# Kernel tuning notes

Measured on AMD Instinct MI355X. Metric: run time of the kernel, lower is better.

## Reference

```python
import jax, jax.numpy as jnp
import numpy as np

N_NODES = 50000
N_EDGES = 800000
D_IN = 96
D_OUT = 96
K_ORDER = 3


def setup_inputs() -> dict:
    key = jax.random.key(0)
    k1, k2, k3, k4, k5 = jax.random.split(key, 5)
    rows = jax.random.randint(k1, (N_EDGES,), 0, N_NODES, dtype=jnp.int64 if jax.config.jax_enable_x64 else jnp.int32)
    cols = jax.random.randint(k2, (N_EDGES,), 0, N_NODES, dtype=jnp.int64 if jax.config.jax_enable_x64 else jnp.int32)
    vals = jax.random.uniform(k3, (N_EDGES,), dtype=jnp.float32) * (1.0 / 16.0)  # ~sym-normalized weights
    H = jax.random.normal(k4, (N_NODES, D_IN), dtype=jnp.float32)
    W = jax.random.normal(k5, (D_IN, D_OUT), dtype=jnp.float32) * (1.0 / np.sqrt(D_IN))
    bias = jnp.zeros((D_OUT,), dtype=jnp.float32)
    return {"rows": rows, "cols": cols, "vals": vals, "H": H, "W": W, "bias": bias}


def reference(rows, cols, vals, H, W, bias):
    n = H.shape[0]

    def spmm(X):  # L @ X via gather-multiply-scatter over COO edges
        return jax.ops.segment_sum(vals[:, None] * X[cols], rows, num_segments=n)

    def ln_mm(X):  # (2L - I) @ X
        return 2.0 * spmm(X) - X

    # k = 0 term: T_0 = H
    H_out = H @ W
    # k = 1 term: T_1 = (2L - I) H  (differentiable, as in torch code)
    T_prev = H
    T_curr = ln_mm(H)
    H_out = H_out + T_curr @ W
    # k >= 2: recurrence computed under no_grad in the original -> stop_gradient
    for _ in range(2, K_ORDER + 1):
        T_next = jax.lax.stop_gradient(2.0 * ln_mm(T_curr) - T_prev)
        H_out = H_out + T_next @ W
        T_prev, T_curr = T_curr, T_next
    return H_out + bias
```

## Files before the change

kernel.cpp:

```cpp
#include <hip/hip_runtime.h>
#include <hip/hip_fp16.h>

#define NN 50000
#define NE 800000
#define D  96
#define NB_SCAN 196

typedef unsigned int   uint32;
typedef unsigned short uint16;
typedef short v8s __attribute__((ext_vector_type(8)));
typedef float v4f __attribute__((ext_vector_type(4)));

__device__ inline uint16 f32_to_bf16(float f) {
    uint32 u = __float_as_uint(f);
    u += 0x7FFF + ((u >> 16) & 1);
    return (uint16)(u >> 16);
}
__device__ inline float bf16_to_f32(uint16 h) {
    return __uint_as_float(((uint32)h) << 16);
}

__global__ void to_bf16(const float4* __restrict__ X, ushort4* __restrict__ Xb, int n4) {
    int i = blockIdx.x * blockDim.x + threadIdx.x;
    if (i < n4) {
        float4 v = X[i];
        ushort4 o;
        o.x = f32_to_bf16(v.x); o.y = f32_to_bf16(v.y);
        o.z = f32_to_bf16(v.z); o.w = f32_to_bf16(v.w);
        Xb[i] = o;
    }
}

__global__ void zero_counts(int* __restrict__ counts) {
    int i = blockIdx.x * blockDim.x + threadIdx.x;
    if (i < NN) counts[i] = 0;
}

__global__ void hist_slots(const int* __restrict__ rows, int* __restrict__ counts,
                           int* __restrict__ slot) {
    int e = blockIdx.x * blockDim.x + threadIdx.x;
    if (e < NE) slot[e] = atomicAdd(&counts[rows[e]], 1);
}

__global__ void scan_p1(const int* __restrict__ counts, int* __restrict__ partials) {
    __shared__ int red[256];
    int t = threadIdx.x;
    int i = blockIdx.x * 256 + t;
    red[t] = (i < NN) ? counts[i] : 0;
    __syncthreads();
    for (int off = 128; off > 0; off >>= 1) {
        if (t < off) red[t] += red[t + off];
        __syncthreads();
    }
    if (t == 0) partials[blockIdx.x] = red[0];
}

__global__ void scan_p2(int* __restrict__ partials) {
    __shared__ int sh[256];
    int t = threadIdx.x;
    int v = (t < NB_SCAN) ? partials[t] : 0;
    sh[t] = v;
    __syncthreads();
    for (int off = 1; off < 256; off <<= 1) {
        int u = (t >= off) ? sh[t - off] : 0;
        __syncthreads();
        sh[t] += u;
        __syncthreads();
    }
    if (t < NB_SCAN) partials[t] = sh[t] - v;
}

__global__ void scan_p3(const int* __restrict__ counts, const int* __restrict__ partials,
                        int* __restrict__ row_ptr) {
    __shared__ int sh[256];
    int t = threadIdx.x;
    int i = blockIdx.x * 256 + t;
    int v = (i < NN) ? counts[i] : 0;
    sh[t] = v;
    __syncthreads();
    for (int off = 1; off < 256; off <<= 1) {
        int u = (t >= off) ? sh[t - off] : 0;
        __syncthreads();
        sh[t] += u;
        __syncthreads();
    }
    int excl = sh[t] - v + partials[blockIdx.x];
    if (i < NN) row_ptr[i] = excl;
    if (i == NN - 1) row_ptr[NN] = excl + v;
}

__global__ void fill_edges(const int* __restrict__ rows, const int* __restrict__ cols,
                           const float* __restrict__ vals, const int* __restrict__ row_ptr,
                           const int* __restrict__ slot, uint32* __restrict__ edges) {
    int e = blockIdx.x * blockDim.x + threadIdx.x;
    if (e < NE) {
        int p = row_ptr[rows[e]] + slot[e];
        __half_raw hr = __half_raw(__float2half(vals[e]));
        edges[p] = (uint32)(cols[e] & 0xFFFF) | ((uint32)hr.x << 16);
    }
}

__global__ void spmm(const int* __restrict__ row_ptr, const uint32* __restrict__ edges,
                     const uint16* __restrict__ Xb, const float* __restrict__ A,
                     const float* __restrict__ B, float* __restrict__ Y,
                     uint16* __restrict__ Yb,
                     float scale, float ca, float cb, int n_nodes) {
    int tid  = threadIdx.x;
    int lane = tid & 31;
    int g    = tid >> 5;
    int r = blockIdx.x * 8 + g;
    if (r >= n_nodes) return;
    bool act = lane < 24;

    float4 acc = make_float4(0.f, 0.f, 0.f, 0.f);
    if (act) {
        float4 av = ((const float4*)(A + (size_t)r * D))[lane];
        float4 bv = ((const float4*)(B + (size_t)r * D))[lane];
        acc.x = ca * av.x + cb * bv.x;
        acc.y = ca * av.y + cb * bv.y;
        acc.z = ca * av.z + cb * bv.z;
        acc.w = ca * av.w + cb * bv.w;
    }

    int s = row_ptr[r];
    int e = row_ptr[r + 1];
    int i = s;
    for (; i + 3 < e; i += 4) {
        uint32 e0 = edges[i], e1 = edges[i+1], e2 = edges[i+2], e3 = edges[i+3];
        ushort4 x0, x1, x2, x3;
        x0.x=x0.y=x0.z=x0.w=0; x1=x0; x2=x0; x3=x0;
        if (act) {
            x0 = ((const ushort4*)(Xb + (size_t)(e0 & 0xFFFF) * D))[lane];
            x1 = ((const ushort4*)(Xb + (size_t)(e1 & 0xFFFF) * D))[lane];
            x2 = ((const ushort4*)(Xb + (size_t)(e2 & 0xFFFF) * D))[lane];
            x3 = ((const ushort4*)(Xb + (size_t)(e3 & 0xFFFF) * D))[lane];
        }
        __half_raw h0, h1, h2, h3;
        h0.x = (uint16)(e0 >> 16); h1.x = (uint16)(e1 >> 16);
        h2.x = (uint16)(e2 >> 16); h3.x = (uint16)(e3 >> 16);
        float v0 = scale * __half2float(__half(h0));
        float v1 = scale * __half2float(__half(h1));
        float v2 = scale * __half2float(__half(h2));
        float v3 = scale * __half2float(__half(h3));
        acc.x += v0*bf16_to_f32(x0.x) + v1*bf16_to_f32(x1.x) + v2*bf16_to_f32(x2.x) + v3*bf16_to_f32(x3.x);
        acc.y += v0*bf16_to_f32(x0.y) + v1*bf16_to_f32(x1.y) + v2*bf16_to_f32(x2.y) + v3*bf16_to_f32(x3.y);
        acc.z += v0*bf16_to_f32(x0.z) + v1*bf16_to_f32(x1.z) + v2*bf16_to_f32(x2.z) + v3*bf16_to_f32(x3.z);
        acc.w += v0*bf16_to_f32(x0.w) + v1*bf16_to_f32(x1.w) + v2*bf16_to_f32(x2.w) + v3*bf16_to_f32(x3.w);
    }
    for (; i < e; ++i) {
        uint32 e0 = edges[i];
        __half_raw h0; h0.x = (uint16)(e0 >> 16);
        float v0 = scale * __half2float(__half(h0));
        if (act) {
            ushort4 x0 = ((const ushort4*)(Xb + (size_t)(e0 & 0xFFFF) * D))[lane];
            acc.x += v0 * bf16_to_f32(x0.x);
            acc.y += v0 * bf16_to_f32(x0.y);
            acc.z += v0 * bf16_to_f32(x0.z);
            acc.w += v0 * bf16_to_f32(x0.w);
        }
    }
    if (act) {
        if (Y) ((float4*)(Y + (size_t)r * D))[lane] = acc;
        if (Yb) {
            ushort4 ob;
            ob.x = f32_to_bf16(acc.x); ob.y = f32_to_bf16(acc.y);
            ob.z = f32_to_bf16(acc.z); ob.w = f32_to_bf16(acc.w);
            ((ushort4*)(Yb + (size_t)r * D))[lane] = ob;
        }
    }
}

__global__ void wfrag_prep(const float* __restrict__ W, uint16* __restrict__ Wfrag) {
    int bt = blockIdx.x;
    int nt = bt / 3, kc = bt % 3;
    int lane = threadIdx.x;
    int col = nt * 16 + (lane & 15);
    int kbase = kc * 32 + (lane >> 4) * 8;
    uint16 tmp[8];
    #pragma unroll
    for (int j = 0; j < 8; ++j) tmp[j] = f32_to_bf16(W[(kbase + j) * D + col]);
    uint32* dst = (uint32*)(Wfrag + ((size_t)bt * 64 + lane) * 8);
    const uint32* src = (const uint32*)tmp;
    #pragma unroll
    for (int j = 0; j < 4; ++j) dst[j] = src[j];
}

__global__ void mfma_gemm(const uint16* __restrict__ Sb, const uint16* __restrict__ Wfrag,
                          const float* __restrict__ bias, float* __restrict__ out) {
    int tid   = threadIdx.x;
    int lane  = tid & 63;
    int wv    = blockIdx.x * (blockDim.x >> 6) + (tid >> 6);
    int nwv   = gridDim.x * (blockDim.x >> 6);
    int col   = lane & 15;
    int quad  = lane >> 4;

    v8s wf[6][3];
    #pragma unroll
    for (int nt = 0; nt < 6; ++nt)
        #pragma unroll
        for (int kc = 0; kc < 3; ++kc)
            wf[nt][kc] = ((const v8s*)Wfrag)[(nt * 3 + kc) * 64 + lane];

    float bi[6];
    #pragma unroll
    for (int nt = 0; nt < 6; ++nt) bi[nt] = bias[nt * 16 + col];

    for (int s = wv; s < NN / 16; s += nwv) {
        int r0 = s * 16;
        const uint16* arow = Sb + (size_t)(r0 + col) * D + quad * 8;
        v8s a0 = *((const v8s*)(arow));
        v8s a1 = *((const v8s*)(arow + 32));
        v8s a2 = *((const v8s*)(arow + 64));
        v4f acc[6];
        #pragma unroll
        for (int nt = 0; nt < 6; ++nt) {
            v4f c = {0.f, 0.f, 0.f, 0.f};
            c = __builtin_amdgcn_mfma_f32_16x16x32_bf16(a0, wf[nt][0], c, 0, 0, 0);
            c = __builtin_amdgcn_mfma_f32_16x16x32_bf16(a1, wf[nt][1], c, 0, 0, 0);
            c = __builtin_amdgcn_mfma_f32_16x16x32_bf16(a2, wf[nt][2], c, 0, 0, 0);
            acc[nt] = c;
        }
        #pragma unroll
        for (int nt = 0; nt < 6; ++nt) {
            float* o = out + (size_t)(r0 + quad * 4) * D + nt * 16 + col;
            o[0 * D] = acc[nt][0] + bi[nt];
            o[1 * D] = acc[nt][1] + bi[nt];
            o[2 * D] = acc[nt][2] + bi[nt];
            o[3 * D] = acc[nt][3] + bi[nt];
        }
    }
}

extern "C" void kernel_launch(void* const* d_in, const int* in_sizes, int n_in,
                              void* d_out, int out_size, void* d_ws, size_t ws_size,
                              hipStream_t stream) {
    const int*   rows = (const int*)d_in[0];
    const int*   cols = (const int*)d_in[1];
    const float* vals = (const float*)d_in[2];
    const float* H    = (const float*)d_in[3];
    const float* W    = (const float*)d_in[4];
    const float* bias = (const float*)d_in[5];
    float* out = (float*)d_out;

    char* ws = (char*)d_ws;
    float*  buf0     = (float*)ws;   ws += (size_t)NN * D * 4;
    float*  T2       = (float*)ws;   ws += (size_t)NN * D * 4;
    uint16* Hb       = (uint16*)ws;  ws += (size_t)NN * D * 2;
    uint16* T1b      = (uint16*)ws;  ws += (size_t)NN * D * 2;
    uint16* T2b      = (uint16*)ws;  ws += (size_t)NN * D * 2;
    uint32* edges    = (uint32*)ws;  ws += (size_t)NE * 4;
    uint16* Wfrag    = (uint16*)ws;  ws += (size_t)18 * 64 * 8 * 2;
    int*    counts   = (int*)ws;     ws += (size_t)NN * 4;
    int*    row_ptr  = (int*)ws;     ws += (size_t)(NN + 1) * 4;
    int*    partials = (int*)ws;     ws += 256 * 4;
    int*    slot     = (int*)buf0;
    float*  T1       = buf0;
    uint16* Sb       = T1b;

    const int nb  = (NN + 255) / 256;
    const int eb  = (NE + 255) / 256;
    const int n4  = NN * D / 4;
    const int cb4 = (n4 + 255) / 256;

    to_bf16<<<cb4, 256, 0, stream>>>((const float4*)H, (ushort4*)Hb, n4);
    wfrag_prep<<<18, 64, 0, stream>>>(W, Wfrag);

    zero_counts<<<nb, 256, 0, stream>>>(counts);
    hist_slots<<<eb, 256, 0, stream>>>(rows, counts, slot);
    scan_p1<<<NB_SCAN, 256, 0, stream>>>(counts, partials);
    scan_p2<<<1, 256, 0, stream>>>(partials);
    scan_p3<<<NB_SCAN, 256, 0, stream>>>(counts, partials, row_ptr);
    fill_edges<<<eb, 256, 0, stream>>>(rows, cols, vals, row_ptr, slot, edges);

    const int sb = (NN + 7) / 8;

    spmm<<<sb, 256, 0, stream>>>(row_ptr, edges, Hb, H, H, T1, T1b, 2.0f, -1.0f, 0.0f, NN);
    spmm<<<sb, 256, 0, stream>>>(row_ptr, edges, T1b, T1, H, T2, T2b, 4.0f, -2.0f, -1.0f, NN);
    spmm<<<sb, 256, 0, stream>>>(row_ptr, edges, T2b, H, T2, (float*)nullptr, Sb, 4.0f, 1.0f, -1.0f, NN);
    mfma_gemm<<<391, 256, 0, stream>>>(Sb, Wfrag, bias, out);
}
```

Baseline: 258.5 us.

## Keep Chebyshev intermediates in bf16 only and merge prep and scan kernels

The three SpMM passes now read their residual operands (H, T1, T2) from the bf16 copies and write only bf16 outputs, so the fp32 intermediate buffers are gone. This roughly halves the dense row traffic per pass. Separately, the H-to-bf16 conversion, count zeroing and W fragment prep are fused into one launch, and scan phases 2 and 3 are merged so each block rescans the partials itself. The cost is extra rounding error, because the recurrence's subtracted terms are now bf16 rather than fp32, and some redundant partial-scan work in every block.

Result: faster. 240.7 us (-6.9%).

```diff
diff --git a/kernel.cpp b/kernel.cpp
--- a/kernel.cpp
+++ b/kernel.cpp
@@ -5,6 +5,9 @@
 #define NE 800000
 #define D  96
 #define NB_SCAN 196
+#define N4 (NN * D / 4)
+#define CB4 ((N4 + 255) / 256)
+#define WFRAG_BLKS 5
 
 typedef unsigned int   uint32;
 typedef unsigned short uint16;
@@ -20,20 +23,39 @@
     return __uint_as_float(((uint32)h) << 16);
 }
 
-__global__ void to_bf16(const float4* __restrict__ X, ushort4* __restrict__ Xb, int n4) {
-    int i = blockIdx.x * blockDim.x + threadIdx.x;
-    if (i < n4) {
-        float4 v = X[i];
-        ushort4 o;
-        o.x = f32_to_bf16(v.x); o.y = f32_to_bf16(v.y);
-        o.z = f32_to_bf16(v.z); o.w = f32_to_bf16(v.w);
-        Xb[i] = o;
-    }
-}
-
-__global__ void zero_counts(int* __restrict__ counts) {
-    int i = blockIdx.x * blockDim.x + threadIdx.x;
-    if (i < NN) counts[i] = 0;
+__global__ void prep(const float4* __restrict__ H, ushort4* __restrict__ Hb,
+                     const float* __restrict__ W, uint16* __restrict__ Wfrag,
+                     int* __restrict__ counts) {
+    int b = blockIdx.x;
+    int t = threadIdx.x;
+    if (b < CB4) {
+        int i = b * 256 + t;
+        if (i < N4) {
+            float4 v = H[i];
+            ushort4 o;
+            o.x = f32_to_bf16(v.x); o.y = f32_to_bf16(v.y);
+            o.z = f32_to_bf16(v.z); o.w = f32_to_bf16(v.w);
+            Hb[i] = o;
+        }
+    } else if (b < CB4 + NB_SCAN) {
+        int i = (b - CB4) * 256 + t;
+        if (i < NN) counts[i] = 0;
+    } else {
+        int idx = (b - CB4 - NB_SCAN) * 256 + t;
+        if (idx < 18 * 64) {
+            int bt = idx >> 6, lane = idx & 63;
+            int nt = bt / 3, kc = bt % 3;
+            int col = nt * 16 + (lane & 15);
+            int kbase = kc * 32 + (lane >> 4) * 8;
+            uint16 tmp[8];
+            #pragma unroll
+            for (int j = 0; j < 8; ++j) tmp[j] = f32_to_bf16(W[(kbase + j) * D + col]);
+            uint32* dst = (uint32*)(Wfrag + ((size_t)bt * 64 + lane) * 8);
+            const uint32* src = (const uint32*)tmp;
+            #pragma unroll
+            for (int j = 0; j < 4; ++j) dst[j] = src[j];
+        }
+    }
 }
 
 __global__ void hist_slots(const int* __restrict__ rows, int* __restrict__ counts,
@@ -55,25 +77,20 @@
     if (t == 0) partials[blockIdx.x] = red[0];
 }
 
-__global__ void scan_p2(int* __restrict__ partials) {
+__global__ void scan_p23(const int* __restrict__ counts, const int* __restrict__ partials,
+                         int* __restrict__ row_ptr) {
+    __shared__ int pp[256];
     __shared__ int sh[256];
     int t = threadIdx.x;
-    int v = (t < NB_SCAN) ? partials[t] : 0;
-    sh[t] = v;
+    pp[t] = (t < NB_SCAN) ? partials[t] : 0;
     __syncthreads();
     for (int off = 1; off < 256; off <<= 1) {
-        int u = (t >= off) ? sh[t - off] : 0;
-        __syncthreads();
-        sh[t] += u;
-        __syncthreads();
-    }
-    if (t < NB_SCAN) partials[t] = sh[t] - v;
-}
-
-__global__ void scan_p3(const int* __restrict__ counts, const int* __restrict__ partials,
-                        int* __restrict__ row_ptr) {
-    __shared__ int sh[256];
-    int t = threadIdx.x;
+        int u = (t >= off) ? pp[t - off] : 0;
+        __syncthreads();
+        pp[t] += u;
+        __syncthreads();
+    }
+    int blk_off = (blockIdx.x == 0) ? 0 : pp[blockIdx.x - 1];
     int i = blockIdx.x * 256 + t;
     int v = (i < NN) ? counts[i] : 0;
     sh[t] = v;
@@ -84,7 +101,7 @@
         sh[t] += u;
         __syncthreads();
     }
-    int excl = sh[t] - v + partials[blockIdx.x];
+    int excl = sh[t] - v + blk_off;
     if (i < NN) row_ptr[i] = excl;
     if (i == NN - 1) row_ptr[NN] = excl + v;
 }
@@ -101,9 +118,8 @@
 }
 
 __global__ void spmm(const int* __restrict__ row_ptr, const uint32* __restrict__ edges,
-                     const uint16* __restrict__ Xb, const float* __restrict__ A,
-                     const float* __restrict__ B, float* __restrict__ Y,
-                     uint16* __restrict__ Yb,
+                     const uint16* __restrict__ Xb, const uint16* __restrict__ A,
+                     const uint16* __restrict__ B, uint16* __restrict__ Yb,
                      float scale, float ca, float cb, int n_nodes) {
     int tid  = threadIdx.x;
     int lane = tid & 31;
@@ -114,12 +130,12 @@
 
     float4 acc = make_float4(0.f, 0.f, 0.f, 0.f);
     if (act) {
-        float4 av = ((const float4*)(A + (size_t)r * D))[lane];
-        float4 bv = ((const float4*)(B + (size_t)r * D))[lane];
-        acc.x = ca * av.x + cb * bv.x;
-        acc.y = ca * av.y + cb * bv.y;
-        acc.z = ca * av.z + cb * bv.z;
-        acc.w = ca * av.w + cb * bv.w;
+        ushort4 av = ((const ushort4*)(A + (size_t)r * D))[lane];
+        ushort4 bv = ((const ushort4*)(B + (size_t)r * D))[lane];
+        acc.x = ca * bf16_to_f32(av.x) + cb * bf16_to_f32(bv.x);
+        acc.y = ca * bf16_to_f32(av.y) + cb * bf16_to_f32(bv.y);
+        acc.z = ca * bf16_to_f32(av.z) + cb * bf16_to_f32(bv.z);
+        acc.w = ca * bf16_to_f32(av.w) + cb * bf16_to_f32(bv.w);
     }
 
     int s = row_ptr[r];
@@ -160,29 +176,11 @@
         }
     }
     if (act) {
-        if (Y) ((float4*)(Y + (size_t)r * D))[lane] = acc;
-        if (Yb) {
-            ushort4 ob;
-            ob.x = f32_to_bf16(acc.x); ob.y = f32_to_bf16(acc.y);
-            ob.z = f32_to_bf16(acc.z); ob.w = f32_to_bf16(acc.w);
-            ((ushort4*)(Yb + (size_t)r * D))[lane] = ob;
-        }
-    }
-}
-
-__global__ void wfrag_prep(const float* __restrict__ W, uint16* __restrict__ Wfrag) {
-    int bt = blockIdx.x;
-    int nt = bt / 3, kc = bt % 3;
-    int lane = threadIdx.x;
-    int col = nt * 16 + (lane & 15);
-    int kbase = kc * 32 + (lane >> 4) * 8;
-    uint16 tmp[8];
-    #pragma unroll
-    for (int j = 0; j < 8; ++j) tmp[j] = f32_to_bf16(W[(kbase + j) * D + col]);
-    uint32* dst = (uint32*)(Wfrag + ((size_t)bt * 64 + lane) * 8);
-    const uint32* src = (const uint32*)tmp;
-    #pragma unroll
-    for (int j = 0; j < 4; ++j) dst[j] = src[j];
+        ushort4 ob;
+        ob.x = f32_to_bf16(acc.x); ob.y = f32_to_bf16(acc.y);
+        ob.z = f32_to_bf16(acc.z); ob.w = f32_to_bf16(acc.w);
+        ((ushort4*)(Yb + (size_t)r * D))[lane] = ob;
+    }
 }
 
 __global__ void mfma_gemm(const uint16* __restrict__ Sb, const uint16* __restrict__ Wfrag,
@@ -243,8 +241,6 @@
     float* out = (float*)d_out;
 
     char* ws = (char*)d_ws;
-    float*  buf0     = (float*)ws;   ws += (size_t)NN * D * 4;
-    float*  T2       = (float*)ws;   ws += (size_t)NN * D * 4;
     uint16* Hb       = (uint16*)ws;  ws += (size_t)NN * D * 2;
     uint16* T1b      = (uint16*)ws;  ws += (size_t)NN * D * 2;
     uint16* T2b      = (uint16*)ws;  ws += (size_t)NN * D * 2;
@@ -253,29 +249,22 @@
     int*    counts   = (int*)ws;     ws += (size_t)NN * 4;
     int*    row_ptr  = (int*)ws;     ws += (size_t)(NN + 1) * 4;
     int*    partials = (int*)ws;     ws += 256 * 4;
-    int*    slot     = (int*)buf0;
-    float*  T1       = buf0;
+    int*    slot     = (int*)T2b;
     uint16* Sb       = T1b;
 
-    const int nb  = (NN + 255) / 256;
-    const int eb  = (NE + 255) / 256;
-    const int n4  = NN * D / 4;
-    const int cb4 = (n4 + 255) / 256;
-
-    to_bf16<<<cb4, 256, 0, stream>>>((const float4*)H, (ushort4*)Hb, n4);
-    wfrag_prep<<<18, 64, 0, stream>>>(W, Wfrag);
-
-    zero_counts<<<nb, 256, 0, stream>>>(counts);
+    const int eb = (NE + 255) / 256;
+
+    prep<<<CB4 + NB_SCAN + WFRAG_BLKS, 256, 0, stream>>>(
+        (const float4*)H, (ushort4*)Hb, W, Wfrag, counts);
     hist_slots<<<eb, 256, 0, stream>>>(rows, counts, slot);
     scan_p1<<<NB_SCAN, 256, 0, stream>>>(counts, partials);
-    scan_p2<<<1, 256, 0, stream>>>(partials);
-    scan_p3<<<NB_SCAN, 256, 0, stream>>>(counts, partials, row_ptr);
+    scan_p23<<<NB_SCAN, 256, 0, stream>>>(counts, partials, row_ptr);
     fill_edges<<<eb, 256, 0, stream>>>(rows, cols, vals, row_ptr, slot, edges);
 
     const int sb = (NN + 7) / 8;
 
-    spmm<<<sb, 256, 0, stream>>>(row_ptr, edges, Hb, H, H, T1, T1b, 2.0f, -1.0f, 0.0f, NN);
-    spmm<<<sb, 256, 0, stream>>>(row_ptr, edges, T1b, T1, H, T2, T2b, 4.0f, -2.0f, -1.0f, NN);
-    spmm<<<sb, 256, 0, stream>>>(row_ptr, edges, T2b, H, T2, (float*)nullptr, Sb, 4.0f, 1.0f, -1.0f, NN);
+    spmm<<<sb, 256, 0, stream>>>(row_ptr, edges, Hb, Hb, Hb, T1b, 2.0f, -1.0f, 0.0f, NN);
+    spmm<<<sb, 256, 0, stream>>>(row_ptr, edges, T1b, T1b, Hb, T2b, 4.0f, -2.0f, -1.0f, NN);
+    spmm<<<sb, 256, 0, stream>>>(row_ptr, edges, T2b, Hb, T2b, Sb, 4.0f, 1.0f, -1.0f, NN);
     mfma_gemm<<<391, 256, 0, stream>>>(Sb, Wfrag, bias, out);
 }
```
